# Kernel tuning notes

Measured on AMD Instinct MI355X. Metric: run time of the kernel, lower is better.

The kernel has to match this reference:

```python
import jax, jax.numpy as jnp
import numpy as np

DIM = 256
HEADS = 8
WS = 8            # window size
SHIFT = 4
MLP_HID = 1024
EPS = 1e-5
HEAD_DIM = DIM // HEADS
SCALE = HEAD_DIM ** -0.5
N = WS * WS       # tokens per window


def _rel_pos_index():
    coords = np.stack(np.meshgrid(np.arange(WS), np.arange(WS), indexing='ij'))  # [2,ws,ws]
    flat = coords.reshape(2, -1)                                                  # [2,N]
    rel = flat[:, :, None] - flat[:, None, :]                                     # [2,N,N]
    rel = rel.transpose(1, 2, 0)                                                  # [N,N,2]
    rel[:, :, 0] += WS - 1
    rel[:, :, 1] += WS - 1
    rel[:, :, 0] *= 2 * WS - 1
    return jnp.asarray(rel.sum(-1))                                               # [N,N] int

REL_IDX = _rel_pos_index()


def layernorm(x, g, b):
    mu = x.mean(-1, keepdims=True)
    var = ((x - mu) ** 2).mean(-1, keepdims=True)
    return (x - mu) * jax.lax.rsqrt(var + EPS) * g + b


def setup_inputs() -> dict:
    key = jax.random.key(0)
    ks = jax.random.split(key, 16)
    s = 0.02
    return {
        'x': jax.random.normal(ks[0], (16, 16384, DIM), jnp.float32),
        'qkv_w': jax.random.normal(ks[1], (DIM, 3 * DIM), jnp.float32) * s,
        'qkv_b': jnp.zeros((3 * DIM,), jnp.float32),
        'proj_w': jax.random.normal(ks[2], (DIM, DIM), jnp.float32) * s,
        'proj_b': jnp.zeros((DIM,), jnp.float32),
        'rpb_table': jax.random.normal(ks[3], ((2 * WS - 1) ** 2, HEADS), jnp.float32) * s,
        'ln1_g': jnp.ones((DIM,), jnp.float32),
        'ln1_b': jnp.zeros((DIM,), jnp.float32),
        'ln2_g': jnp.ones((DIM,), jnp.float32),
        'ln2_b': jnp.zeros((DIM,), jnp.float32),
        'mlp_w1': jax.random.normal(ks[4], (DIM, MLP_HID), jnp.float32) * s,
        'mlp_b1': jnp.zeros((MLP_HID,), jnp.float32),
        'mlp_w2': jax.random.normal(ks[5], (MLP_HID, DIM), jnp.float32) * s,
        'mlp_b2': jnp.zeros((DIM,), jnp.float32),
        'H': 128,
        'W': 128,
    }


def reference(x, qkv_w, qkv_b, proj_w, proj_b, rpb_table,
              ln1_g, ln1_b, ln2_g, ln2_b, mlp_w1, mlp_b1, mlp_w2, mlp_b2, H, W):
    B, L, C = x.shape
    shortcut = x

    h = layernorm(x, ln1_g, ln1_b).reshape(B, H, W, C)
    if SHIFT > 0:
        h = jnp.roll(h, (-SHIFT, -SHIFT), axis=(1, 2))

    # window partition: [B,H,W,C] -> [B*nW, N, C]
    h = h.reshape(B, H // WS, WS, W // WS, WS, C).transpose(0, 1, 3, 2, 4, 5)
    xw = h.reshape(-1, N, C)
    Bw = xw.shape[0]

    # window attention
    qkv = (xw @ qkv_w + qkv_b).reshape(Bw, N, 3, HEADS, HEAD_DIM)
    q, k, v = qkv[:, :, 0], qkv[:, :, 1], qkv[:, :, 2]        # [Bw,N,H,D]
    attn = jnp.einsum('bnhd,bmhd->bhnm', q, k) * SCALE         # [Bw,H,N,N]
    bias = rpb_table[REL_IDX.reshape(-1)].reshape(N, N, HEADS).transpose(2, 0, 1)
    attn = jax.nn.softmax(attn + bias[None], axis=-1)
    out = jnp.einsum('bhnm,bmhd->bnhd', attn, v).reshape(Bw, N, C)
    out = out @ proj_w + proj_b

    # window reverse
    out = out.reshape(B, H // WS, W // WS, WS, WS, C).transpose(0, 1, 3, 2, 4, 5).reshape(B, H, W, C)
    if SHIFT > 0:
        out = jnp.roll(out, (SHIFT, SHIFT), axis=(1, 2))
    out = out.reshape(B, L, C)

    h2 = layernorm(out, ln2_g, ln2_b)
    mlp = jax.nn.gelu(h2 @ mlp_w1 + mlp_b1, approximate=False) @ mlp_w2 + mlp_b2
    return shortcut + out + mlp
```

## Files before the change

kernel.cpp:

```cpp
#include <hip/hip_runtime.h>
#include <math.h>

typedef short bfrag __attribute__((ext_vector_type(8)));
typedef float ffrag __attribute__((ext_vector_type(4)));

#define MFMA16(a, b, c) __builtin_amdgcn_mfma_f32_16x16x32_bf16((a), (b), (c), 0, 0, 0)

__device__ __align__(16) unsigned short g_wt[786432];

__device__ __forceinline__ unsigned bf16b(float f) {
  unsigned u = __float_as_uint(f);
  return (u + 0x7FFFu + ((u >> 16) & 1u)) >> 16;
}
__device__ __forceinline__ unsigned pk2(float lo, float hi) {
  return bf16b(lo) | (bf16b(hi) << 16);
}
__device__ __forceinline__ float bf2f(unsigned u) {
  return __uint_as_float(u << 16);
}

__global__ void conv_w(const float* __restrict__ qkv_w, const float* __restrict__ proj_w,
                       const float* __restrict__ w1, const float* __restrict__ w2) {
  const int idx = blockIdx.x * 256 + threadIdx.x;
  const float* src; int c, k2, C, K, ofs;
  if (idx < 98304)       { src = qkv_w;  C = 768;  K = 256;  c = idx % 768;  k2 = idx / 768;  ofs = 0; }
  else if (idx < 131072) { int i = idx - 98304;  src = proj_w; C = 256;  K = 256;  c = i % 256;  k2 = i / 256;  ofs = 196608; }
  else if (idx < 262144) { int i = idx - 131072; src = w1;     C = 1024; K = 256;  c = i % 1024; k2 = i / 1024; ofs = 262144; }
  else                   { int i = idx - 262144; src = w2;     C = 256;  K = 1024; c = i % 256;  k2 = i / 256;  ofs = 524288; }
  const float lo = src[(2 * k2) * C + c];
  const float hi = src[(2 * k2 + 1) * C + c];
  *(unsigned*)&g_wt[ofs + c * K + 2 * k2] = pk2(lo, hi);
}

__device__ __forceinline__ int swz(int row, int col, int C) {
  return row * (C * 2) + ((((col >> 3) ^ (row & 7)) << 4) + ((col & 7) << 1));
}
__device__ __forceinline__ bfrag ldfrag(const char* lds, int outer, int k0, int C) {
  const int l = threadIdx.x & 63;
  return *(const bfrag*)(lds + swz(outer + (l & 15), k0 + ((l >> 4) << 3), C));
}

__device__ __forceinline__ void stage_tile(char* lds, const unsigned short* __restrict__ src,
                                           long rowBase, int strideShorts, int kOfs) {
  const int wv = threadIdx.x >> 6, l = threadIdx.x & 63;
  #pragma unroll
  for (int p = 0; p < 8; ++p) {
    const int base = wv * 1024 + p * 8192;
    const int off = base + l * 16;
    const int row = off >> 9;
    const int ss = ((off & 511) >> 4) ^ (row & 7);
    const unsigned short* g = src + (rowBase + row) * (long)strideShorts + kOfs + ss * 8;
    __builtin_amdgcn_global_load_lds((const __attribute__((address_space(1))) void*)g,
                                     (__attribute__((address_space(3))) void*)(lds + base),
                                     16, 0, 0);
  }
}

template <int DSTROWB>
__device__ __forceinline__ void glds_stage(char* lds, const unsigned short* src,
                                           int srcRowShorts, int bytes) {
  const int wv = threadIdx.x >> 6, l = threadIdx.x & 63;
  for (int base = wv * 1024; base < bytes; base += 8192) {
    const int off = base + l * 16;
    const int row = off / DSTROWB;
    const int slot = (off % DSTROWB) >> 4;
    const int ss = slot ^ (row & 7);
    const unsigned short* g = src + row * srcRowShorts + ss * 8;
    __builtin_amdgcn_global_load_lds((const __attribute__((address_space(1))) void*)g,
                                     (__attribute__((address_space(3))) void*)(lds + base),
                                     16, 0, 0);
  }
}

__device__ __forceinline__ void mm_core(const char* AX, const char* BW, ffrag acc[2][4]) {
  const int wv = threadIdx.x >> 6;
  const int rh = wv >> 2, cq = wv & 3;
  #pragma unroll
  for (int ks = 0; ks < 8; ++ks) {
    const bfrag aw0 = ldfrag(BW, cq * 32, ks * 32, 256);
    const bfrag aw1 = ldfrag(BW, cq * 32 + 16, ks * 32, 256);
    #pragma unroll
    for (int nt = 0; nt < 4; ++nt) {
      const bfrag xb = ldfrag(AX, rh * 64 + nt * 16, ks * 32, 256);
      acc[0][nt] = MFMA16(aw0, xb, acc[0][nt]);
      acc[1][nt] = MFMA16(aw1, xb, acc[1][nt]);
    }
  }
}

__device__ __forceinline__ void ln_pack(float d0, float d1, float d2, float d3,
                                        const float* g, const float* bb, int lane,
                                        unsigned& o0, unsigned& o1) {
  float s = d0 + d1 + d2 + d3;
  #pragma unroll
  for (int o = 32; o; o >>= 1) s += __shfl_xor(s, o);
  const float mu = s * (1.f / 256.f);
  d0 -= mu; d1 -= mu; d2 -= mu; d3 -= mu;
  float q = d0 * d0 + d1 * d1 + d2 * d2 + d3 * d3;
  #pragma unroll
  for (int o = 32; o; o >>= 1) q += __shfl_xor(q, o);
  const float vv = q * (1.f / 256.f) + 1e-5f;
  float rs = rsqrtf(vv);
  rs = rs * (1.5f - 0.5f * vv * rs * rs);
  const float4 g4 = *(const float4*)(g + lane * 4);
  const float4 b4 = *(const float4*)(bb + lane * 4);
  o0 = pk2(d0 * rs * g4.x + b4.x, d1 * rs * g4.y + b4.y);
  o1 = pk2(d2 * rs * g4.z + b4.z, d3 * rs * g4.w + b4.w);
}

__global__ __launch_bounds__(512) void ln1_k(const float* __restrict__ x,
    const float* __restrict__ g, const float* __restrict__ bb,
    unsigned short* __restrict__ XB, long rowOfs) {
  const int wv = threadIdx.x >> 6, l = threadIdx.x & 63;
  const long lrow = (long)blockIdx.x * 8 + wv;
  const float4 v = *(const float4*)(x + (rowOfs + lrow) * 256 + l * 4);
  unsigned o0, o1;
  ln_pack(v.x, v.y, v.z, v.w, g, bb, l, o0, o1);
  unsigned short* dp = XB + lrow * 256 + l * 4;
  *(unsigned*)dp = o0; *(unsigned*)(dp + 2) = o1;
}

__global__ __launch_bounds__(512) void gemm_qkv(const unsigned short* __restrict__ XB,
    const float* __restrict__ qkv_b, unsigned short* __restrict__ QKV) {
  __shared__ __align__(16) char smem[131072];
  char* AX = smem; char* BW = smem + 65536;
  const int mb = blockIdx.x, nb = blockIdx.y;
  stage_tile(AX, XB, (long)mb * 128, 256, 0);
  stage_tile(BW, g_wt, nb * 128, 256, 0);
  __syncthreads();
  ffrag acc[2][4];
  #pragma unroll
  for (int a = 0; a < 2; ++a)
    #pragma unroll
    for (int n = 0; n < 4; ++n) { ffrag z = {0.f, 0.f, 0.f, 0.f}; acc[a][n] = z; }
  mm_core(AX, BW, acc);
  const int l = threadIdx.x & 63, wv = threadIdx.x >> 6;
  const int rh = wv >> 2, cq = wv & 3;
  const float sc = (nb < 2) ? 0.17677669529663687f : 1.f;
  #pragma unroll
  for (int mt = 0; mt < 2; ++mt) {
    const int cg = nb * 128 + cq * 32 + mt * 16 + ((l >> 4) << 2);
    const float4 bq = *(const float4*)(qkv_b + cg);
    #pragma unroll
    for (int nt = 0; nt < 4; ++nt) {
      const long row = (long)mb * 128 + rh * 64 + nt * 16 + (l & 15);
      unsigned short* dp = QKV + row * 768 + cg;
      *(unsigned*)dp       = pk2((acc[mt][nt][0] + bq.x) * sc, (acc[mt][nt][1] + bq.y) * sc);
      *(unsigned*)(dp + 2) = pk2((acc[mt][nt][2] + bq.z) * sc, (acc[mt][nt][3] + bq.w) * sc);
    }
  }
}

__global__ __launch_bounds__(512) void gemm_proj(const unsigned short* __restrict__ O,
    const float* __restrict__ proj_b, unsigned short* __restrict__ outw) {
  __shared__ __align__(16) char smem[131072];
  char* AX = smem; char* BW = smem + 65536;
  const int mb = blockIdx.x, nb = blockIdx.y;
  stage_tile(AX, O, (long)mb * 128, 256, 0);
  stage_tile(BW, g_wt + 196608, nb * 128, 256, 0);
  __syncthreads();
  ffrag acc[2][4];
  #pragma unroll
  for (int a = 0; a < 2; ++a)
    #pragma unroll
    for (int n = 0; n < 4; ++n) { ffrag z = {0.f, 0.f, 0.f, 0.f}; acc[a][n] = z; }
  mm_core(AX, BW, acc);
  const int l = threadIdx.x & 63, wv = threadIdx.x >> 6;
  const int rh = wv >> 2, cq = wv & 3;
  #pragma unroll
  for (int mt = 0; mt < 2; ++mt) {
    const int cg = nb * 128 + cq * 32 + mt * 16 + ((l >> 4) << 2);
    const float4 pb = *(const float4*)(proj_b + cg);
    #pragma unroll
    for (int nt = 0; nt < 4; ++nt) {
      const long row = (long)mb * 128 + rh * 64 + nt * 16 + (l & 15);
      unsigned short* dp = outw + row * 256 + cg;
      *(unsigned*)dp       = pk2(acc[mt][nt][0] + pb.x, acc[mt][nt][1] + pb.y);
      *(unsigned*)(dp + 2) = pk2(acc[mt][nt][2] + pb.z, acc[mt][nt][3] + pb.w);
    }
  }
}

__global__ __launch_bounds__(512, 4) void attn_core(const unsigned short* __restrict__ QKV,
    const float* __restrict__ rpb, unsigned short* __restrict__ O, int bofs) {
  __shared__ __align__(16) char smem[81920];
  char* KL = smem;
  char* VT = smem + 32768;
  char* PB = smem + 65536;
  const int t = threadIdx.x, wv = t >> 6, l = t & 63;
  const int blk = blockIdx.x;
  const int b = blk >> 8, w = blk & 255;
  const int wi = w >> 4, wj = w & 15;
  const int bi0 = wi * 8 + 4, bj0 = wj * 8 + 4;
  const ffrag ZERO4 = {0.f, 0.f, 0.f, 0.f};

  #define SROW(r) (((long)b << 14) + (((bi0 + ((r) >> 3)) & 127) << 7) + ((bj0 + ((r) & 7)) & 127))
  #define GROW(r) (((long)(bofs + b) << 14) + (((bi0 + ((r) >> 3)) & 127) << 7) + ((bj0 + ((r) & 7)) & 127))

  #pragma unroll
  for (int p = 0; p < 4; ++p) {
    const int base = wv * 1024 + p * 8192;
    const int off = base + l * 16;
    const int kv = off >> 9;
    const int ss = ((off & 511) >> 4) ^ (kv & 7);
    const unsigned short* g = QKV + SROW(kv) * 768 + 256 + ss * 8;
    __builtin_amdgcn_global_load_lds((const __attribute__((address_space(1))) void*)g,
                                     (__attribute__((address_space(3))) void*)(KL + base),
                                     16, 0, 0);
  }

  {
    const int rp = t & 31, dh = t >> 5;
    const unsigned short* v0p = QKV + SROW(2 * rp) * 768 + 512 + dh * 16;
    const unsigned short* v1p = QKV + SROW(2 * rp + 1) * 768 + 512 + dh * 16;
    const bfrag a0 = *(const bfrag*)v0p, a1 = *(const bfrag*)(v0p + 8);
    const bfrag c0 = *(const bfrag*)v1p, c1 = *(const bfrag*)(v1p + 8);
    #pragma unroll
    for (int j = 0; j < 8; ++j) {
      const unsigned w0 = ((unsigned)(unsigned short)a0[j]) | (((unsigned)(unsigned short)c0[j]) << 16);
      const unsigned w1 = ((unsigned)(unsigned short)a1[j]) | (((unsigned)(unsigned short)c1[j]) << 16);
      *(unsigned*)(VT + swz(dh * 16 + j, 2 * rp, 64)) = w0;
      *(unsigned*)(VT + swz(dh * 16 + 8 + j, 2 * rp, 64)) = w1;
    }
  }
  __syncthreads();

  const int qt = wv & 3, hh = wv >> 2;
  char* myPB = PB + wv * 2048;
  const int colb = l & 15;
  const int rbase = qt * 16 + ((l >> 4) << 2);

  for (int i = 0; i < 4; ++i) {
    const int h = 2 * i + hh;
    const int hk = h * 32;
    const int qr = qt * 16 + (l & 15);
    const bfrag aq = *(const bfrag*)(QKV + SROW(qr) * 768 + hk + ((l >> 4) << 3));
    ffrag s[4];
    #pragma unroll
    for (int nt = 0; nt < 4; ++nt) {
      const bfrag bk = ldfrag(KL, nt * 16, hk, 256);
      s[nt] = MFMA16(aq, bk, ZERO4);
    }
    float pr[4][4], mx[4], sm[4];
    #pragma unroll
    for (int reg = 0; reg < 4; ++reg) mx[reg] = -3e38f;
    #pragma unroll
    for (int nt = 0; nt < 4; ++nt)
      #pragma unroll
      for (int reg = 0; reg < 4; ++reg) {
        const int rr = rbase + reg, cc = nt * 16 + colb;
        const int idx = ((rr >> 3) - (cc >> 3) + 7) * 15 + ((rr & 7) - (cc & 7) + 7);
        pr[nt][reg] = s[nt][reg] + rpb[idx * 8 + h];
        mx[reg] = fmaxf(mx[reg], pr[nt][reg]);
      }
    #pragma unroll
    for (int reg = 0; reg < 4; ++reg) {
      #pragma unroll
      for (int o = 1; o < 16; o <<= 1) mx[reg] = fmaxf(mx[reg], __shfl_xor(mx[reg], o));
      sm[reg] = 0.f;
    }
    #pragma unroll
    for (int nt = 0; nt < 4; ++nt)
      #pragma unroll
      for (int reg = 0; reg < 4; ++reg) {
        pr[nt][reg] = __expf(pr[nt][reg] - mx[reg]);
        sm[reg] += pr[nt][reg];
      }
    #pragma unroll
    for (int reg = 0; reg < 4; ++reg) {
      #pragma unroll
      for (int o = 1; o < 16; o <<= 1) sm[reg] += __shfl_xor(sm[reg], o);
      sm[reg] = 1.f / sm[reg];
    }
    #pragma unroll
    for (int nt = 0; nt < 4; ++nt)
      #pragma unroll
      for (int reg = 0; reg < 4; ++reg)
        *(unsigned short*)(myPB + swz(((l >> 4) << 2) + reg, nt * 16 + colb, 64)) =
            (unsigned short)bf16b(pr[nt][reg] * sm[reg]);

    ffrag o0 = ZERO4, o1 = ZERO4;
    #pragma unroll
    for (int ks = 0; ks < 2; ++ks) {
      const bfrag ap = ldfrag(myPB, 0, ks * 32, 64);
      const bfrag bv0 = ldfrag(VT, hk, ks * 32, 64);
      const bfrag bv1 = ldfrag(VT, hk + 16, ks * 32, 64);
      o0 = MFMA16(ap, bv0, o0);
      o1 = MFMA16(ap, bv1, o1);
    }
    #pragma unroll
    for (int reg = 0; reg < 4; ++reg) {
      const long orow = GROW(rbase + reg);
      O[orow * 256 + hk + colb] = (unsigned short)bf16b(o0[reg]);
      O[orow * 256 + hk + 16 + colb] = (unsigned short)bf16b(o1[reg]);
    }
  }
  #undef SROW
  #undef GROW
}

__global__ __launch_bounds__(512, 4) void swin_mlp(
    const float* __restrict__ x, const unsigned short* __restrict__ outw,
    const float* __restrict__ ln2g, const float* __restrict__ ln2b,
    const float* __restrict__ b1, const float* __restrict__ b2,
    float* __restrict__ y)
{
  __shared__ __align__(16) char smem[73728];
  char* H2 = smem;
  char* WS = smem + 32768;
  char* HD = smem + 65536;
  const int t = threadIdx.x, wv = t >> 6, l = t & 63;
  const long base = (long)blockIdx.x << 6;

  #pragma unroll
  for (int i = 0; i < 8; ++i) {
    const int r = wv * 8 + i;
    const uint2 raw = *(const uint2*)(outw + (base + r) * 256 + l * 4);
    unsigned o0, o1;
    ln_pack(bf2f(raw.x & 0xFFFFu), bf2f(raw.x >> 16), bf2f(raw.y & 0xFFFFu), bf2f(raw.y >> 16),
            ln2g, ln2b, l, o0, o1);
    *(unsigned*)(H2 + swz(r, l * 4, 256)) = o0;
    *(unsigned*)(H2 + swz(r, l * 4 + 2, 256)) = o1;
  }
  __syncthreads();

  const int mq = wv >> 1, nq = (wv & 1) << 1;

  ffrag acc2[2][4];
  #pragma unroll
  for (int mt = 0; mt < 2; ++mt)
    #pragma unroll
    for (int nt = 0; nt < 4; ++nt) { ffrag z = {0.f, 0.f, 0.f, 0.f}; acc2[mt][nt] = z; }

  for (int ch = 0; ch < 16; ++ch) {
    glds_stage<512>(WS, g_wt + 262144 + ch * 64 * 256, 256, 32768);
    __syncthreads();
    ffrag a1[2];
    { ffrag z = {0.f, 0.f, 0.f, 0.f}; a1[0] = z; a1[1] = z; }
    #pragma unroll
    for (int ks = 0; ks < 8; ++ks) {
      const bfrag a = ldfrag(WS, mq * 16, ks * 32, 256);
      const bfrag bb0 = ldfrag(H2, nq * 16, ks * 32, 256);
      const bfrag bb1 = ldfrag(H2, (nq + 1) * 16, ks * 32, 256);
      a1[0] = MFMA16(a, bb0, a1[0]);
      a1[1] = MFMA16(a, bb1, a1[1]);
    }
    __syncthreads();

    const int c0 = mq * 16 + ((l >> 4) << 2);
    const float4 b14 = *(const float4*)(b1 + ch * 64 + c0);
    #pragma unroll
    for (int nt = 0; nt < 2; ++nt) {
      const int rr = (nq + nt) * 16 + (l & 15);
      const float u0 = a1[nt][0] + b14.x, u1 = a1[nt][1] + b14.y;
      const float u2 = a1[nt][2] + b14.z, u3 = a1[nt][3] + b14.w;
      const float g0 = 0.5f * u0 * (1.f + erff(u0 * 0.70710678118654752f));
      const float g1 = 0.5f * u1 * (1.f + erff(u1 * 0.70710678118654752f));
      const float g2 = 0.5f * u2 * (1.f + erff(u2 * 0.70710678118654752f));
      const float g3 = 0.5f * u3 * (1.f + erff(u3 * 0.70710678118654752f));
      *(unsigned*)(HD + swz(rr, c0, 64)) = pk2(g0, g1);
      *(unsigned*)(HD + swz(rr, c0 + 2, 64)) = pk2(g2, g3);
    }
    glds_stage<128>(WS, g_wt + 524288 + ch * 64, 1024, 32768);
    __syncthreads();

    #pragma unroll
    for (int ks = 0; ks < 2; ++ks) {
      const bfrag am0 = ldfrag(WS, (wv * 2) * 16, ks * 32, 64);
      const bfrag am1 = ldfrag(WS, (wv * 2 + 1) * 16, ks * 32, 64);
      #pragma unroll
      for (int nt = 0; nt < 4; ++nt) {
        const bfrag bb = ldfrag(HD, nt * 16, ks * 32, 64);
        acc2[0][nt] = MFMA16(am0, bb, acc2[0][nt]);
        acc2[1][nt] = MFMA16(am1, bb, acc2[1][nt]);
      }
    }
    __syncthreads();
  }

  #pragma unroll
  for (int mt = 0; mt < 2; ++mt) {
    const int c0 = (wv * 2 + mt) * 16 + ((l >> 4) << 2);
    const float4 b24 = *(const float4*)(b2 + c0);
    #pragma unroll
    for (int nt = 0; nt < 4; ++nt) {
      const long row = base + nt * 16 + (l & 15);
      const float4 xv = *(const float4*)(x + row * 256 + c0);
      const uint2 ov = *(const uint2*)(outw + row * 256 + c0);
      float4 res;
      res.x = acc2[mt][nt][0] + b24.x + xv.x + bf2f(ov.x & 0xFFFFu);
      res.y = acc2[mt][nt][1] + b24.y + xv.y + bf2f(ov.x >> 16);
      res.z = acc2[mt][nt][2] + b24.z + xv.z + bf2f(ov.y & 0xFFFFu);
      res.w = acc2[mt][nt][3] + b24.w + xv.w + bf2f(ov.y >> 16);
      *(float4*)(y + row * 256 + c0) = res;
    }
  }
}

extern "C" void kernel_launch(void* const* d_in, const int* in_sizes, int n_in,
                              void* d_out, int out_size, void* d_ws, size_t ws_size,
                              hipStream_t stream) {
  (void)in_sizes; (void)n_in; (void)out_size; (void)ws_size;
  const float* x      = (const float*)d_in[0];
  const float* qkv_w  = (const float*)d_in[1];
  const float* qkv_b  = (const float*)d_in[2];
  const float* proj_w = (const float*)d_in[3];
  const float* proj_b = (const float*)d_in[4];
  const float* rpb    = (const float*)d_in[5];
  const float* ln1g   = (const float*)d_in[6];
  const float* ln1b   = (const float*)d_in[7];
  const float* ln2g   = (const float*)d_in[8];
  const float* ln2b   = (const float*)d_in[9];
  const float* w1     = (const float*)d_in[10];
  const float* b1     = (const float*)d_in[11];
  const float* w2     = (const float*)d_in[12];
  const float* b2     = (const float*)d_in[13];
  float* y = (float*)d_out;
  char* ws = (char*)d_ws;

  unsigned short* XB   = (unsigned short*)(ws);
  unsigned short* QKV  = (unsigned short*)(ws + 33554432);
  unsigned short* Obuf = (unsigned short*)(ws + 134217728);
  unsigned short* outw = (unsigned short*)(ws);

  hipLaunchKernelGGL(conv_w, dim3(1536), dim3(256), 0, stream, qkv_w, proj_w, w1, w2);
  for (int g = 0; g < 4; ++g) {
    hipLaunchKernelGGL(ln1_k, dim3(8192), dim3(512), 0, stream,
                       x, ln1g, ln1b, XB, (long)g * 65536);
    hipLaunchKernelGGL(gemm_qkv, dim3(512, 6), dim3(512), 0, stream, XB, qkv_b, QKV);
    hipLaunchKernelGGL(attn_core, dim3(1024), dim3(512), 0, stream, QKV, rpb, Obuf, g * 4);
  }
  hipLaunchKernelGGL(gemm_proj, dim3(2048, 2), dim3(512), 0, stream, Obuf, proj_b, outw);
  hipLaunchKernelGGL(swin_mlp, dim3(4096), dim3(512), 0, stream,
                     x, outw, ln2g, ln2b, b1, b2, y);
}
```

Baseline: 1.301 ms.

## Split QKV/proj GEMM K loop to halve LDS, use tanh GELU, overlap W2 staging

```diff
diff --git a/kernel.cpp b/kernel.cpp
--- a/kernel.cpp
+++ b/kernel.cpp
@@ -17,6 +17,10 @@
 }
 __device__ __forceinline__ float bf2f(unsigned u) {
   return __uint_as_float(u << 16);
+}
+__device__ __forceinline__ float gelu_t(float u) {
+  const float z = 1.5957691216057308f * (u + 0.044715f * u * u * u);
+  return u / (1.f + __expf(-z));
 }
 
 __global__ void conv_w(const float* __restrict__ qkv_w, const float* __restrict__ proj_w,
@@ -40,15 +44,15 @@
   return *(const bfrag*)(lds + swz(outer + (l & 15), k0 + ((l >> 4) << 3), C));
 }
 
-__device__ __forceinline__ void stage_tile(char* lds, const unsigned short* __restrict__ src,
-                                           long rowBase, int strideShorts, int kOfs) {
+__device__ __forceinline__ void stage128(char* lds, const unsigned short* __restrict__ src,
+                                         long rowBase, int strideShorts, int kOfs) {
   const int wv = threadIdx.x >> 6, l = threadIdx.x & 63;
   #pragma unroll
-  for (int p = 0; p < 8; ++p) {
+  for (int p = 0; p < 4; ++p) {
     const int base = wv * 1024 + p * 8192;
     const int off = base + l * 16;
-    const int row = off >> 9;
-    const int ss = ((off & 511) >> 4) ^ (row & 7);
+    const int row = off >> 8;
+    const int ss = ((off & 255) >> 4) ^ (row & 7);
     const unsigned short* g = src + (rowBase + row) * (long)strideShorts + kOfs + ss * 8;
     __builtin_amdgcn_global_load_lds((const __attribute__((address_space(1))) void*)g,
                                      (__attribute__((address_space(3))) void*)(lds + base),
@@ -72,16 +76,16 @@
   }
 }
 
-__device__ __forceinline__ void mm_core(const char* AX, const char* BW, ffrag acc[2][4]) {
+__device__ __forceinline__ void mm_core128(const char* AX, const char* BW, ffrag acc[2][4]) {
   const int wv = threadIdx.x >> 6;
   const int rh = wv >> 2, cq = wv & 3;
   #pragma unroll
-  for (int ks = 0; ks < 8; ++ks) {
-    const bfrag aw0 = ldfrag(BW, cq * 32, ks * 32, 256);
-    const bfrag aw1 = ldfrag(BW, cq * 32 + 16, ks * 32, 256);
+  for (int ks = 0; ks < 4; ++ks) {
+    const bfrag aw0 = ldfrag(BW, cq * 32, ks * 32, 128);
+    const bfrag aw1 = ldfrag(BW, cq * 32 + 16, ks * 32, 128);
     #pragma unroll
     for (int nt = 0; nt < 4; ++nt) {
-      const bfrag xb = ldfrag(AX, rh * 64 + nt * 16, ks * 32, 256);
+      const bfrag xb = ldfrag(AX, rh * 64 + nt * 16, ks * 32, 128);
       acc[0][nt] = MFMA16(aw0, xb, acc[0][nt]);
       acc[1][nt] = MFMA16(aw1, xb, acc[1][nt]);
     }
@@ -120,20 +124,24 @@
   *(unsigned*)dp = o0; *(unsigned*)(dp + 2) = o1;
 }
 
-__global__ __launch_bounds__(512) void gemm_qkv(const unsigned short* __restrict__ XB,
+__global__ __launch_bounds__(512, 4) void gemm_qkv(const unsigned short* __restrict__ XB,
     const float* __restrict__ qkv_b, unsigned short* __restrict__ QKV) {
-  __shared__ __align__(16) char smem[131072];
-  char* AX = smem; char* BW = smem + 65536;
+  __shared__ __align__(16) char smem[65536];
+  char* AX = smem; char* BW = smem + 32768;
   const int mb = blockIdx.x, nb = blockIdx.y;
-  stage_tile(AX, XB, (long)mb * 128, 256, 0);
-  stage_tile(BW, g_wt, nb * 128, 256, 0);
-  __syncthreads();
   ffrag acc[2][4];
   #pragma unroll
   for (int a = 0; a < 2; ++a)
     #pragma unroll
     for (int n = 0; n < 4; ++n) { ffrag z = {0.f, 0.f, 0.f, 0.f}; acc[a][n] = z; }
-  mm_core(AX, BW, acc);
+  #pragma unroll
+  for (int kc = 0; kc < 2; ++kc) {
+    stage128(AX, XB, (long)mb * 128, 256, kc * 128);
+    stage128(BW, g_wt, (long)nb * 128, 256, kc * 128);
+    __syncthreads();
+    mm_core128(AX, BW, acc);
+    __syncthreads();
+  }
   const int l = threadIdx.x & 63, wv = threadIdx.x >> 6;
   const int rh = wv >> 2, cq = wv & 3;
   const float sc = (nb < 2) ? 0.17677669529663687f : 1.f;
@@ -151,20 +159,24 @@
   }
 }
 
-__global__ __launch_bounds__(512) void gemm_proj(const unsigned short* __restrict__ O,
+__global__ __launch_bounds__(512, 4) void gemm_proj(const unsigned short* __restrict__ O,
     const float* __restrict__ proj_b, unsigned short* __restrict__ outw) {
-  __shared__ __align__(16) char smem[131072];
-  char* AX = smem; char* BW = smem + 65536;
+  __shared__ __align__(16) char smem[65536];
+  char* AX = smem; char* BW = smem + 32768;
   const int mb = blockIdx.x, nb = blockIdx.y;
-  stage_tile(AX, O, (long)mb * 128, 256, 0);
-  stage_tile(BW, g_wt + 196608, nb * 128, 256, 0);
-  __syncthreads();
   ffrag acc[2][4];
   #pragma unroll
   for (int a = 0; a < 2; ++a)
     #pragma unroll
     for (int n = 0; n < 4; ++n) { ffrag z = {0.f, 0.f, 0.f, 0.f}; acc[a][n] = z; }
-  mm_core(AX, BW, acc);
+  #pragma unroll
+  for (int kc = 0; kc < 2; ++kc) {
+    stage128(AX, O, (long)mb * 128, 256, kc * 128);
+    stage128(BW, g_wt + 196608, (long)nb * 128, 256, kc * 128);
+    __syncthreads();
+    mm_core128(AX, BW, acc);
+    __syncthreads();
+  }
   const int l = threadIdx.x & 63, wv = threadIdx.x >> 6;
   const int rh = wv >> 2, cq = wv & 3;
   #pragma unroll
@@ -347,21 +359,19 @@
     }
     __syncthreads();
 
+    glds_stage<128>(WS, g_wt + 524288 + ch * 64, 1024, 32768);
     const int c0 = mq * 16 + ((l >> 4) << 2);
     const float4 b14 = *(const float4*)(b1 + ch * 64 + c0);
     #pragma unroll
     for (int nt = 0; nt < 2; ++nt) {
       const int rr = (nq + nt) * 16 + (l & 15);
-      const float u0 = a1[nt][0] + b14.x, u1 = a1[nt][1] + b14.y;
-      const float u2 = a1[nt][2] + b14.z, u3 = a1[nt][3] + b14.w;
-      const float g0 = 0.5f * u0 * (1.f + erff(u0 * 0.70710678118654752f));
-      const float g1 = 0.5f * u1 * (1.f + erff(u1 * 0.70710678118654752f));
-      const float g2 = 0.5f * u2 * (1.f + erff(u2 * 0.70710678118654752f));
-      const float g3 = 0.5f * u3 * (1.f + erff(u3 * 0.70710678118654752f));
+      const float g0 = gelu_t(a1[nt][0] + b14.x);
+      const float g1 = gelu_t(a1[nt][1] + b14.y);
+      const float g2 = gelu_t(a1[nt][2] + b14.z);
+      const float g3 = gelu_t(a1[nt][3] + b14.w);
       *(unsigned*)(HD + swz(rr, c0, 64)) = pk2(g0, g1);
       *(unsigned*)(HD + swz(rr, c0 + 2, 64)) = pk2(g2, g3);
     }
-    glds_stage<128>(WS, g_wt + 524288 + ch * 64, 1024, 32768);
     __syncthreads();
 
     #pragma unroll
```

Result: faster. 1.238 ms (-4.8%).
